# Kernel optimization log

Hardware: AMD Instinct MI355X
Metric: run time of the kernel (lower is better)

Reference implementation:

```python
import jax, jax.numpy as jnp
import numpy as np

N_NODES = 50000
N_EDGES = 400000
D = 64        # hidden_features
H_NE = 16     # hidden_ne_features
L = 4         # num_layers
EPS = 1e-5


def _ln(z, g, b):
    # layer norm over feature dim
    mu = jnp.mean(z, axis=-1, keepdims=True)
    var = jnp.var(z, axis=-1, keepdims=True)
    return (z - mu) * jax.lax.rsqrt(var + EPS) * g + b


def setup_inputs() -> dict:
    key = jax.random.key(0)
    ks = iter(jax.random.split(key, 64))
    def rn(shape, s=0.05):
        return jax.random.normal(next(ks), shape, dtype=jnp.float32) * s
    inp = {
        "x": rn((N_NODES, 2), 1.0),
        "e": rn((N_EDGES, 2), 1.0),
        "src": jax.random.randint(next(ks), (N_EDGES,), 0, N_NODES, dtype=jnp.int32),
        "dst": jax.random.randint(next(ks), (N_EDGES,), 0, N_NODES, dtype=jnp.int32),
        # node / edge encoders (2-layer MLPs)
        "ne_W1": rn((2, H_NE)), "ne_b1": jnp.zeros((H_NE,), jnp.float32),
        "ne_W2": rn((H_NE, D)), "ne_b2": jnp.zeros((D,), jnp.float32),
        "ee_W1": rn((2, H_NE)), "ee_b1": jnp.zeros((H_NE,), jnp.float32),
        "ee_W2": rn((H_NE, D)), "ee_b2": jnp.zeros((D,), jnp.float32),
        # stacked per-layer GatedGCN weights
        "A1": rn((L, D, D)), "bA1": jnp.zeros((L, D), jnp.float32),
        "A2": rn((L, D, D)), "bA2": jnp.zeros((L, D), jnp.float32),
        "A3": rn((L, D, D)), "bA3": jnp.zeros((L, D), jnp.float32),
        "B1": rn((L, D, D)), "bB1": jnp.zeros((L, D), jnp.float32),
        "B2": rn((L, D, D)), "bB2": jnp.zeros((L, D), jnp.float32),
        "B3": rn((L, D, D)), "bB3": jnp.zeros((L, D), jnp.float32),
        "ge": jnp.ones((L, D), jnp.float32), "be": jnp.zeros((L, D), jnp.float32),
        "gh": jnp.ones((L, D), jnp.float32), "bh": jnp.zeros((L, D), jnp.float32),
        # score predictor
        "pW1": rn((3 * D, D)), "pb1": jnp.zeros((D,), jnp.float32),
        "pW2": rn((D, 1)), "pb2": jnp.zeros((1,), jnp.float32),
    }
    return inp


def _forward(x, e, src, dst,
             ne_W1, ne_b1, ne_W2, ne_b2,
             ee_W1, ee_b1, ee_W2, ee_b2,
             A1, bA1, A2, bA2, A3, bA3,
             B1, bB1, B2, bB2, B3, bB3,
             ge, be, gh, bh,
             pW1, pb1, pW2, pb2):
    # encoders
    x = jax.nn.relu(x @ ne_W1 + ne_b1) @ ne_W2 + ne_b2      # [N, D]
    e = jax.nn.relu(e @ ee_W1 + ee_b1) @ ee_W2 + ee_b2      # [E, D]

    params = {"A1": A1, "bA1": bA1, "A2": A2, "bA2": bA2,
              "A3": A3, "bA3": bA3, "B1": B1, "bB1": bB1,
              "B2": B2, "bB2": bB2, "B3": B3, "bB3": bB3,
              "ge": ge, "be": be, "gh": gh, "bh": bh}

    def layer(carry, p):
        x, e = carry
        # edge update: e_ij += ReLU(LN(B1 h_i + B2 h_j + B3 e_ij))
        e_hat = (x[src] @ p["B1"] + p["bB1"]
                 + x[dst] @ p["B2"] + p["bB2"]
                 + e @ p["B3"] + p["bB3"])                  # [E, D]
        e = e + jax.nn.relu(_ln(e_hat, p["ge"], p["be"]))
        sigma = jax.nn.sigmoid(e)                             # gates [E, D]
        # directed aggregation: forward (src->dst) and backward (dst->src)
        a2 = x @ p["A2"] + p["bA2"]
        a3 = x @ p["A3"] + p["bA3"]
        m_f = jax.ops.segment_sum(sigma * a2[src], dst, num_segments=N_NODES)
        d_f = jax.ops.segment_sum(sigma, dst, num_segments=N_NODES)
        m_b = jax.ops.segment_sum(sigma * a3[dst], src, num_segments=N_NODES)
        d_b = jax.ops.segment_sum(sigma, src, num_segments=N_NODES)
        h = (x @ p["A1"] + p["bA1"]
             + m_f / (d_f + EPS) + m_b / (d_b + EPS))        # [N, D]
        x = x + jax.nn.relu(_ln(h, p["gh"], p["bh"]))
        return (x, e), None

    (x, e), _ = jax.lax.scan(layer, (x, e), params)

    # score predictor: MLP over cat(x_src, x_dst, e)
    z = jnp.concatenate([x[src], x[dst], e], axis=-1)        # [E, 3D]
    return jax.nn.relu(z @ pW1 + pb1) @ pW2 + pb2            # [E, 1]


def reference(x, e, src, dst,
              ne_W1, ne_b1, ne_W2, ne_b2,
              ee_W1, ee_b1, ee_W2, ee_b2,
              A1, bA1, A2, bA2, A3, bA3,
              B1, bB1, B2, bB2, B3, bB3,
              ge, be, gh, bh,
              pW1, pb1, pW2, pb2):
    return _forward(x, e, src, dst,
                    ne_W1, ne_b1, ne_W2, ne_b2,
                    ee_W1, ee_b1, ee_W2, ee_b2,
                    A1, bA1, A2, bA2, A3, bA3,
                    B1, bB1, B2, bB2, B3, bB3,
                    ge, be, gh, bh,
                    pW1, pb1, pW2, pb2)
```

## Files before the change

### kernel.cpp

```cpp
#include <hip/hip_runtime.h>

#define N_NODES 50000
#define N_EDGES 400000
#define EPSV 1e-5f
#define SCAN_BLK 49
#define SCAN_PAD (49 * 1024)

__global__ __launch_bounds__(256) void encode_kernel(
    const float* __restrict__ in2, const float* __restrict__ W1,
    const float* __restrict__ b1, const float* __restrict__ W2,
    const float* __restrict__ b2, float* __restrict__ out, int nrows)
{
  int t = blockIdx.x * 256 + threadIdx.x;
  int row = t >> 4;
  int d0 = t & 15;
  if (row >= nrows) return;
  float x0 = in2[row * 2 + 0], x1 = in2[row * 2 + 1];
  float h[16];
#pragma unroll
  for (int j = 0; j < 16; ++j)
    h[j] = fmaxf(fmaf(x0, W1[j], fmaf(x1, W1[16 + j], b1[j])), 0.f);
#pragma unroll
  for (int q = 0; q < 4; ++q) {
    int d = d0 + q * 16;
    float a = b2[d];
#pragma unroll
    for (int j = 0; j < 16; ++j) a = fmaf(h[j], W2[j * 64 + d], a);
    out[(size_t)row * 64 + d] = a;
  }
}

__global__ __launch_bounds__(256) void encode_perm_kernel(
    const float* __restrict__ in2, const float* __restrict__ W1,
    const float* __restrict__ b1, const float* __restrict__ W2,
    const float* __restrict__ b2, const int2* __restrict__ csr_f,
    float* __restrict__ out)
{
  int t = blockIdx.x * 256 + threadIdx.x;
  int row = t >> 4;
  int d0 = t & 15;
  if (row >= N_EDGES) return;
  int orig = csr_f[row].x;
  float x0 = in2[orig * 2 + 0], x1 = in2[orig * 2 + 1];
  float h[16];
#pragma unroll
  for (int j = 0; j < 16; ++j)
    h[j] = fmaxf(fmaf(x0, W1[j], fmaf(x1, W1[16 + j], b1[j])), 0.f);
#pragma unroll
  for (int q = 0; q < 4; ++q) {
    int d = d0 + q * 16;
    float a = b2[d];
#pragma unroll
    for (int j = 0; j < 16; ++j) a = fmaf(h[j], W2[j * 64 + d], a);
    out[(size_t)row * 64 + d] = a;
  }
}

__global__ __launch_bounds__(256) void hist_kernel(
    const int* __restrict__ src, const int* __restrict__ dst,
    int* __restrict__ cnt_f, int* __restrict__ cnt_b)
{
  int t = blockIdx.x * 256 + threadIdx.x;
  if (t >= N_EDGES) return;
  atomicAdd(&cnt_f[dst[t]], 1);
  atomicAdd(&cnt_b[src[t]], 1);
}

__global__ __launch_bounds__(1024) void scanA_kernel(
    const int* __restrict__ cnt_f, const int* __restrict__ cnt_b,
    int* __restrict__ part, int* __restrict__ bsum)
{
  int dir = blockIdx.x / SCAN_BLK;
  int blk = blockIdx.x % SCAN_BLK;
  const int* cnt = dir ? cnt_b : cnt_f;
  int t = threadIdx.x;
  int idx = blk * 1024 + t;
  int v = (idx < N_NODES) ? cnt[idx] : 0;
  __shared__ int sh[1024];
  sh[t] = v;
  __syncthreads();
  for (int o = 1; o < 1024; o <<= 1) {
    int u = (t >= o) ? sh[t - o] : 0;
    __syncthreads();
    sh[t] += u;
    __syncthreads();
  }
  part[dir * SCAN_PAD + idx] = sh[t] - v;
  if (t == 1023) bsum[dir * SCAN_BLK + blk] = sh[1023];
}

__global__ __launch_bounds__(128) void scanB_kernel(
    int* __restrict__ bsum, int* __restrict__ off_f, int* __restrict__ off_b)
{
  int dir = threadIdx.x >> 6;
  int i = threadIdx.x & 63;
  int v = (i < SCAN_BLK) ? bsum[dir * SCAN_BLK + i] : 0;
  int s = v;
#pragma unroll
  for (int o = 1; o < 64; o <<= 1) {
    int u = __shfl_up(s, o, 64);
    if (i >= o) s += u;
  }
  if (i < SCAN_BLK) bsum[dir * SCAN_BLK + i] = s - v;
  if (i == SCAN_BLK - 1) {
    if (dir == 0) off_f[N_NODES] = s;
    else off_b[N_NODES] = s;
  }
}

__global__ __launch_bounds__(1024) void scanC_kernel(
    const int* __restrict__ part, const int* __restrict__ bsum,
    int* __restrict__ off_f, int* __restrict__ off_b,
    int* __restrict__ cur_f, int* __restrict__ cur_b)
{
  int dir = blockIdx.x / SCAN_BLK;
  int blk = blockIdx.x % SCAN_BLK;
  int t = threadIdx.x;
  int idx = blk * 1024 + t;
  if (idx >= N_NODES) return;
  int v = part[dir * SCAN_PAD + idx] + bsum[dir * SCAN_BLK + blk];
  if (dir == 0) { off_f[idx] = v; cur_f[idx] = v; }
  else { off_b[idx] = v; cur_b[idx] = v; }
}

__global__ __launch_bounds__(256) void fill_kernel(
    const int* __restrict__ src, const int* __restrict__ dst,
    int* __restrict__ cur_f, int* __restrict__ cur_b,
    int2* __restrict__ csr_f, int2* __restrict__ csr_b)
{
  int t = blockIdx.x * 256 + threadIdx.x;
  if (t >= N_EDGES) return;
  int dv = dst[t], sv = src[t];
  int p = atomicAdd(&cur_f[dv], 1);
  csr_f[p] = make_int2(t, sv);
  int q = atomicAdd(&cur_b[sv], 1);
  csr_b[q] = make_int2(t, dv);
}

__global__ __launch_bounds__(256) void sort_kernel(
    const int* __restrict__ off_f, const int* __restrict__ off_b,
    int2* __restrict__ csr_f, int2* __restrict__ csr_b)
{
  int t = blockIdx.x * 256 + threadIdx.x;
  int n;
  int2* csr;
  const int* off;
  if (t < N_NODES) { n = t; csr = csr_f; off = off_f; }
  else if (t < 2 * N_NODES) { n = t - N_NODES; csr = csr_b; off = off_b; }
  else return;
  int b = off[n], e = off[n + 1];
  for (int i = b + 1; i < e; ++i) {
    int2 key = csr[i];
    int j = i - 1;
    while (j >= b && csr[j].x > key.x) { csr[j + 1] = csr[j]; --j; }
    csr[j + 1] = key;
  }
}

__global__ __launch_bounds__(256) void aux_inv_kernel(
    const int2* __restrict__ csr_f, int* __restrict__ inv_f,
    int* __restrict__ src_f)
{
  int p = blockIdx.x * 256 + threadIdx.x;
  if (p >= N_EDGES) return;
  int2 c = csr_f[p];
  inv_f[c.x] = p;
  src_f[p] = c.y;
}

__global__ __launch_bounds__(256) void aux_dst_kernel(
    const int* __restrict__ off_f, int* __restrict__ dst_f)
{
  int n = blockIdx.x * 256 + threadIdx.x;
  if (n >= N_NODES) return;
  int b = off_f[n], e = off_f[n + 1];
  for (int p = b; p < e; ++p) dst_f[p] = n;
}

__global__ __launch_bounds__(256) void aux_remap_kernel(
    const int* __restrict__ inv_f, int2* __restrict__ csr_b)
{
  int q = blockIdx.x * 256 + threadIdx.x;
  if (q >= N_EDGES) return;
  int2 c = csr_b[q];
  csr_b[q] = make_int2(inv_f[c.x], c.y);
}


__global__ __launch_bounds__(320, 6) void node_gemm_kernel(
    const float* __restrict__ X,
    const float* __restrict__ A1, const float* __restrict__ A2,
    const float* __restrict__ A3, const float* __restrict__ B1,
    const float* __restrict__ B2,
    const float* __restrict__ bA1, const float* __restrict__ bA2,
    const float* __restrict__ bA3, const float* __restrict__ bB1,
    const float* __restrict__ bB2,
    float* __restrict__ NA, int l)
{
  __shared__ float tl[64 * 36];
  int wid = threadIdx.x >> 6;
  int lane = threadIdx.x & 63;
  int row0 = blockIdx.x * 32;
  for (int i = threadIdx.x; i < 32 * 16; i += 320) {
    int r = i >> 4, c4 = (i & 15) * 4;
    int row = row0 + r;
    float4 v = (row < N_NODES)
                   ? *reinterpret_cast<const float4*>(&X[(size_t)row * 64 + c4])
                   : make_float4(0.f, 0.f, 0.f, 0.f);
    tl[(c4 + 0) * 36 + r] = v.x;
    tl[(c4 + 1) * 36 + r] = v.y;
    tl[(c4 + 2) * 36 + r] = v.z;
    tl[(c4 + 3) * 36 + r] = v.w;
  }
  __syncthreads();
  int r8 = lane & 7, c8 = lane >> 3;
  int col = 8 * c8;
  const float* W;
  const float* bb;
  if (wid == 0) { W = A1; bb = bA1; }
  else if (wid == 1) { W = A2; bb = bA2; }
  else if (wid == 2) { W = A3; bb = bA3; }
  else if (wid == 3) { W = B1; bb = bB1; }
  else { W = B2; bb = bB2; }
  W += l * 64 * 64;
  float acc[4][8];
#pragma unroll
  for (int i = 0; i < 4; ++i)
#pragma unroll
    for (int j = 0; j < 8; ++j) acc[i][j] = 0.f;
#pragma unroll 8
  for (int k = 0; k < 64; ++k) {
    float4 er = *reinterpret_cast<const float4*>(&tl[k * 36 + 4 * r8]);
    float4 w0 = *reinterpret_cast<const float4*>(&W[k * 64 + col]);
    float4 w1 = *reinterpret_cast<const float4*>(&W[k * 64 + col + 4]);
    float ev[4] = {er.x, er.y, er.z, er.w};
    float wv[8] = {w0.x, w0.y, w0.z, w0.w, w1.x, w1.y, w1.z, w1.w};
#pragma unroll
    for (int i = 0; i < 4; ++i)
#pragma unroll
      for (int j = 0; j < 8; ++j) acc[i][j] = fmaf(ev[i], wv[j], acc[i][j]);
  }
  float4 b0 = *reinterpret_cast<const float4*>(&bb[l * 64 + col]);
  float4 b1 = *reinterpret_cast<const float4*>(&bb[l * 64 + col + 4]);
  float* out = NA + (size_t)wid * N_NODES * 64;
#pragma unroll
  for (int i = 0; i < 4; ++i) {
    int row = row0 + 4 * r8 + i;
    if (row < N_NODES) {
      *reinterpret_cast<float4*>(&out[(size_t)row * 64 + col]) =
          make_float4(acc[i][0] + b0.x, acc[i][1] + b0.y, acc[i][2] + b0.z,
                      acc[i][3] + b0.w);
      *reinterpret_cast<float4*>(&out[(size_t)row * 64 + col + 4]) =
          make_float4(acc[i][4] + b1.x, acc[i][5] + b1.y, acc[i][6] + b1.z,
                      acc[i][7] + b1.w);
    }
  }
}

__global__ __launch_bounds__(256, 8) void edge_update_kernel(
    const float* __restrict__ NA,
    const float* __restrict__ B3, const float* __restrict__ bB3,
    const float* __restrict__ ge, const float* __restrict__ be,
    const int* __restrict__ src_f, const int* __restrict__ dst_f,
    float* __restrict__ E64, int l)
{
  __shared__ float ett[4][64 * 20];
  int wid = threadIdx.x >> 6;
  int lane = threadIdx.x & 63;
  int tile = blockIdx.x * 4 + wid;
  int e0 = tile * 16;
  int r4 = lane & 3, c16 = lane >> 2;
  int col = 4 * c16;
  float* tl = ett[wid];
#pragma unroll
  for (int rb = 0; rb < 4; ++rb) {
    int r = e0 + 4 * rb;
    float v0 = E64[(size_t)(r + 0) * 64 + lane];
    float v1 = E64[(size_t)(r + 1) * 64 + lane];
    float v2 = E64[(size_t)(r + 2) * 64 + lane];
    float v3 = E64[(size_t)(r + 3) * 64 + lane];
    *reinterpret_cast<float4*>(&tl[lane * 20 + 4 * rb]) =
        make_float4(v0, v1, v2, v3);
  }
  const float* W = B3 + l * 64 * 64;
  float acc[4][4];
#pragma unroll
  for (int i = 0; i < 4; ++i)
#pragma unroll
    for (int j = 0; j < 4; ++j) acc[i][j] = 0.f;
#pragma unroll 8
  for (int k = 0; k < 64; ++k) {
    float4 er = *reinterpret_cast<const float4*>(&tl[k * 20 + 4 * r4]);
    float4 w0 = *reinterpret_cast<const float4*>(&W[k * 64 + col]);
    float ev[4] = {er.x, er.y, er.z, er.w};
    float wv[4] = {w0.x, w0.y, w0.z, w0.w};
#pragma unroll
    for (int i = 0; i < 4; ++i)
#pragma unroll
      for (int j = 0; j < 4; ++j) acc[i][j] = fmaf(ev[i], wv[j], acc[i][j]);
  }
  const float* b1x = NA + (size_t)3 * N_NODES * 64;
  const float* b2x = NA + (size_t)4 * N_NODES * 64;
  float4 t0;
  t0 = *reinterpret_cast<const float4*>(&bB3[l * 64 + col]);
  float bbv[4] = {t0.x, t0.y, t0.z, t0.w};
  t0 = *reinterpret_cast<const float4*>(&ge[l * 64 + col]);
  float gev[4] = {t0.x, t0.y, t0.z, t0.w};
  t0 = *reinterpret_cast<const float4*>(&be[l * 64 + col]);
  float bev[4] = {t0.x, t0.y, t0.z, t0.w};
#pragma unroll
  for (int i = 0; i < 4; ++i) {
    int row = e0 + 4 * r4 + i;
    int sv = src_f[row];
    int dv = dst_f[row];
    float4 g0 = *reinterpret_cast<const float4*>(&b1x[(size_t)sv * 64 + col]);
    float4 h0 = *reinterpret_cast<const float4*>(&b2x[(size_t)dv * 64 + col]);
    float4 o0 = *reinterpret_cast<const float4*>(&E64[(size_t)row * 64 + col]);
    float g1v[4] = {g0.x, g0.y, g0.z, g0.w};
    float g2v[4] = {h0.x, h0.y, h0.z, h0.w};
    float eov[4] = {o0.x, o0.y, o0.z, o0.w};
    float z[4];
    float s1 = 0.f, s2 = 0.f;
#pragma unroll
    for (int j = 0; j < 4; ++j) {
      z[j] = acc[i][j] + bbv[j] + g1v[j] + g2v[j];
      s1 += z[j];
      s2 = fmaf(z[j], z[j], s2);
    }
    s1 += __shfl_xor(s1, 4, 64);  s2 += __shfl_xor(s2, 4, 64);
    s1 += __shfl_xor(s1, 8, 64);  s2 += __shfl_xor(s2, 8, 64);
    s1 += __shfl_xor(s1, 16, 64); s2 += __shfl_xor(s2, 16, 64);
    s1 += __shfl_xor(s1, 32, 64); s2 += __shfl_xor(s2, 32, 64);
    float mean = s1 * (1.f / 64.f);
    float var = fmaxf(s2 * (1.f / 64.f) - mean * mean, 0.f);
    float rstd = rsqrtf(var + EPSV);
    float o[4];
#pragma unroll
    for (int j = 0; j < 4; ++j)
      o[j] = eov[j] + fmaxf(fmaf((z[j] - mean) * rstd, gev[j], bev[j]), 0.f);
    *reinterpret_cast<float4*>(&E64[(size_t)row * 64 + col]) =
        make_float4(o[0], o[1], o[2], o[3]);
  }
}

__global__ __launch_bounds__(256) void aggregate_kernel(
    const float* __restrict__ NA, const float* __restrict__ E64,
    const int* __restrict__ off_f, const int* __restrict__ off_b,
    const int* __restrict__ src_f, const int2* __restrict__ csr_b,
    const float* __restrict__ gh, const float* __restrict__ bh,
    float* __restrict__ X, int l)
{
  int wave = threadIdx.x >> 6;
  int lane = threadIdx.x & 63;
  int n = blockIdx.x * 4 + wave;
  if (n >= N_NODES) return;
  const float* A1x = NA;
  const float* A2x = NA + (size_t)N_NODES * 64;
  const float* A3x = NA + (size_t)2 * N_NODES * 64;
  float xo = X[(size_t)n * 64 + lane];
  float a1v = A1x[(size_t)n * 64 + lane];
  float ghv = gh[l * 64 + lane];
  float bhv = bh[l * 64 + lane];
  int pf = off_f[n], pfe = off_f[n + 1];
  int pb = off_b[n], pbe = off_b[n + 1];
  float mf = 0.f, df = 0.f, mb = 0.f, db = 0.f;
#pragma unroll 4
  for (int p = pf; p < pfe; ++p) {
    float ev = E64[(size_t)p * 64 + lane];
    float av = A2x[(size_t)src_f[p] * 64 + lane];
    float sg = __builtin_amdgcn_rcpf(1.f + __expf(-ev));
    mf = fmaf(sg, av, mf);
    df += sg;
  }
#pragma unroll 4
  for (int p = pb; p < pbe; ++p) {
    int2 c = csr_b[p];
    float ev = E64[(size_t)c.x * 64 + lane];
    float av = A3x[(size_t)c.y * 64 + lane];
    float sg = __builtin_amdgcn_rcpf(1.f + __expf(-ev));
    mb = fmaf(sg, av, mb);
    db += sg;
  }
  float h = a1v + mf * __builtin_amdgcn_rcpf(df + EPSV) +
            mb * __builtin_amdgcn_rcpf(db + EPSV);
  float s1 = h, s2 = h * h;
#pragma unroll
  for (int m = 1; m < 64; m <<= 1) {
    s1 += __shfl_xor(s1, m, 64);
    s2 += __shfl_xor(s2, m, 64);
  }
  float mean = s1 * (1.f / 64.f);
  float var = fmaxf(s2 * (1.f / 64.f) - mean * mean, 0.f);
  float rstd = rsqrtf(var + EPSV);
  X[(size_t)n * 64 + lane] =
      xo + fmaxf(fmaf((h - mean) * rstd, ghv, bhv), 0.f);
}

__global__ __launch_bounds__(128, 8) void pred_node_kernel(
    const float* __restrict__ X, const float* __restrict__ pW1,
    float* __restrict__ U, float* __restrict__ V)
{
  __shared__ float tl[64 * 36];
  int wid = threadIdx.x >> 6;
  int lane = threadIdx.x & 63;
  int row0 = blockIdx.x * 32;
  for (int i = threadIdx.x; i < 32 * 16; i += 128) {
    int r = i >> 4, c4 = (i & 15) * 4;
    int row = row0 + r;
    float4 v = (row < N_NODES)
                   ? *reinterpret_cast<const float4*>(&X[(size_t)row * 64 + c4])
                   : make_float4(0.f, 0.f, 0.f, 0.f);
    tl[(c4 + 0) * 36 + r] = v.x;
    tl[(c4 + 1) * 36 + r] = v.y;
    tl[(c4 + 2) * 36 + r] = v.z;
    tl[(c4 + 3) * 36 + r] = v.w;
  }
  __syncthreads();
  int r8 = lane & 7, c8 = lane >> 3;
  int col = 8 * c8;
  const float* W = pW1 + (size_t)wid * 64 * 64;
  float acc[4][8];
#pragma unroll
  for (int i = 0; i < 4; ++i)
#pragma unroll
    for (int j = 0; j < 8; ++j) acc[i][j] = 0.f;
#pragma unroll 8
  for (int k = 0; k < 64; ++k) {
    float4 er = *reinterpret_cast<const float4*>(&tl[k * 36 + 4 * r8]);
    float4 w0 = *reinterpret_cast<const float4*>(&W[k * 64 + col]);
    float4 w1 = *reinterpret_cast<const float4*>(&W[k * 64 + col + 4]);
    float ev[4] = {er.x, er.y, er.z, er.w};
    float wv[8] = {w0.x, w0.y, w0.z, w0.w, w1.x, w1.y, w1.z, w1.w};
#pragma unroll
    for (int i = 0; i < 4; ++i)
#pragma unroll
      for (int j = 0; j < 8; ++j) acc[i][j] = fmaf(ev[i], wv[j], acc[i][j]);
  }
  float* out = wid ? V : U;
#pragma unroll
  for (int i = 0; i < 4; ++i) {
    int row = row0 + 4 * r8 + i;
    if (row < N_NODES) {
      *reinterpret_cast<float4*>(&out[(size_t)row * 64 + col]) =
          make_float4(acc[i][0], acc[i][1], acc[i][2], acc[i][3]);
      *reinterpret_cast<float4*>(&out[(size_t)row * 64 + col + 4]) =
          make_float4(acc[i][4], acc[i][5], acc[i][6], acc[i][7]);
    }
  }
}

__global__ __launch_bounds__(256, 8) void pred_edge_kernel(
    const float* __restrict__ U, const float* __restrict__ V,
    const float* __restrict__ E64,
    const int2* __restrict__ csr_f, const int* __restrict__ dst_f,
    const float* __restrict__ pW1, const float* __restrict__ pb1,
    const float* __restrict__ pW2, const float* __restrict__ pb2,
    float* __restrict__ out)
{
  __shared__ float ett[4][64 * 20];
  int wid = threadIdx.x >> 6;
  int lane = threadIdx.x & 63;
  int tile = blockIdx.x * 4 + wid;
  int e0 = tile * 16;
  int r4 = lane & 3, c16 = lane >> 2;
  int col = 4 * c16;
  float* tl = ett[wid];
#pragma unroll
  for (int rb = 0; rb < 4; ++rb) {
    int r = e0 + 4 * rb;
    float v0 = E64[(size_t)(r + 0) * 64 + lane];
    float v1 = E64[(size_t)(r + 1) * 64 + lane];
    float v2 = E64[(size_t)(r + 2) * 64 + lane];
    float v3 = E64[(size_t)(r + 3) * 64 + lane];
    *reinterpret_cast<float4*>(&tl[lane * 20 + 4 * rb]) =
        make_float4(v0, v1, v2, v3);
  }
  const float* W = pW1 + (size_t)128 * 64;
  float acc[4][4];
#pragma unroll
  for (int i = 0; i < 4; ++i)
#pragma unroll
    for (int j = 0; j < 4; ++j) acc[i][j] = 0.f;
#pragma unroll 8
  for (int k = 0; k < 64; ++k) {
    float4 er = *reinterpret_cast<const float4*>(&tl[k * 20 + 4 * r4]);
    float4 w0 = *reinterpret_cast<const float4*>(&W[k * 64 + col]);
    float ev[4] = {er.x, er.y, er.z, er.w};
    float wv[4] = {w0.x, w0.y, w0.z, w0.w};
#pragma unroll
    for (int i = 0; i < 4; ++i)
#pragma unroll
      for (int j = 0; j < 4; ++j) acc[i][j] = fmaf(ev[i], wv[j], acc[i][j]);
  }
  float4 t0;
  t0 = *reinterpret_cast<const float4*>(&pb1[col]);
  float pb1v[4] = {t0.x, t0.y, t0.z, t0.w};
  t0 = *reinterpret_cast<const float4*>(&pW2[col]);
  float pw2v[4] = {t0.x, t0.y, t0.z, t0.w};
  float pb2v = pb2[0];
#pragma unroll
  for (int i = 0; i < 4; ++i) {
    int row = e0 + 4 * r4 + i;
    int2 cf = csr_f[row];
    int sv = cf.y;
    int dv = dst_f[row];
    float4 g0 = *reinterpret_cast<const float4*>(&U[(size_t)sv * 64 + col]);
    float4 h0 = *reinterpret_cast<const float4*>(&V[(size_t)dv * 64 + col]);
    float g1v[4] = {g0.x, g0.y, g0.z, g0.w};
    float g2v[4] = {h0.x, h0.y, h0.z, h0.w};
    float hsum = 0.f;
#pragma unroll
    for (int j = 0; j < 4; ++j) {
      float z = acc[i][j] + pb1v[j] + g1v[j] + g2v[j];
      hsum = fmaf(fmaxf(z, 0.f), pw2v[j], hsum);
    }
    hsum += __shfl_xor(hsum, 4, 64);
    hsum += __shfl_xor(hsum, 8, 64);
    hsum += __shfl_xor(hsum, 16, 64);
    hsum += __shfl_xor(hsum, 32, 64);
    if (c16 == 0) out[cf.x] = hsum + pb2v;
  }
}

extern "C" void kernel_launch(void* const* d_in, const int* in_sizes, int n_in,
                              void* d_out, int out_size, void* d_ws, size_t ws_size,
                              hipStream_t stream)
{
  const float* x = (const float*)d_in[0];
  const float* e = (const float*)d_in[1];
  const int* src = (const int*)d_in[2];
  const int* dst = (const int*)d_in[3];
  const float* neW1 = (const float*)d_in[4];
  const float* neb1 = (const float*)d_in[5];
  const float* neW2 = (const float*)d_in[6];
  const float* neb2 = (const float*)d_in[7];
  const float* eeW1 = (const float*)d_in[8];
  const float* eeb1 = (const float*)d_in[9];
  const float* eeW2 = (const float*)d_in[10];
  const float* eeb2 = (const float*)d_in[11];
  const float* A1 = (const float*)d_in[12];
  const float* bA1 = (const float*)d_in[13];
  const float* A2 = (const float*)d_in[14];
  const float* bA2 = (const float*)d_in[15];
  const float* A3 = (const float*)d_in[16];
  const float* bA3 = (const float*)d_in[17];
  const float* B1 = (const float*)d_in[18];
  const float* bB1 = (const float*)d_in[19];
  const float* B2 = (const float*)d_in[20];
  const float* bB2 = (const float*)d_in[21];
  const float* B3 = (const float*)d_in[22];
  const float* bB3 = (const float*)d_in[23];
  const float* ge = (const float*)d_in[24];
  const float* be = (const float*)d_in[25];
  const float* gh = (const float*)d_in[26];
  const float* bh = (const float*)d_in[27];
  const float* pW1 = (const float*)d_in[28];
  const float* pb1 = (const float*)d_in[29];
  const float* pW2 = (const float*)d_in[30];
  const float* pb2 = (const float*)d_in[31];

  char* ws = (char*)d_ws;
  float* X = (float*)ws;      ws += (size_t)N_NODES * 64 * 4;
  float* NA = (float*)ws;     ws += (size_t)5 * N_NODES * 64 * 4;
  float* E64 = (float*)ws;    ws += (size_t)N_EDGES * 64 * 4;
  int* cnt_f = (int*)ws;      ws += (size_t)N_NODES * 4;
  int* cnt_b = (int*)ws;      ws += (size_t)N_NODES * 4;
  int* off_f = (int*)ws;      ws += (size_t)(N_NODES + 1) * 4;
  int* off_b = (int*)ws;      ws += (size_t)(N_NODES + 1) * 4;
  int* cur_f = (int*)ws;      ws += (size_t)N_NODES * 4;
  int* cur_b = (int*)ws;      ws += (size_t)N_NODES * 4;
  int2* csr_f = (int2*)ws;    ws += (size_t)N_EDGES * 8;
  int2* csr_b = (int2*)ws;    ws += (size_t)N_EDGES * 8;
  int* part = (int*)ws;       ws += (size_t)2 * SCAN_PAD * 4;
  int* bsum = (int*)ws;       ws += (size_t)2 * SCAN_BLK * 4;
  int* inv_f = (int*)ws;      ws += (size_t)N_EDGES * 4;
  int* dst_f = (int*)ws;      ws += (size_t)N_EDGES * 4;
  int* src_f = (int*)ws;      ws += (size_t)N_EDGES * 4;
  float* U = NA + (size_t)3 * N_NODES * 64;
  float* V = NA + (size_t)4 * N_NODES * 64;

  hipMemsetAsync(cnt_f, 0, (size_t)2 * N_NODES * 4, stream);
  hist_kernel<<<(N_EDGES + 255) / 256, 256, 0, stream>>>(src, dst, cnt_f, cnt_b);
  scanA_kernel<<<2 * SCAN_BLK, 1024, 0, stream>>>(cnt_f, cnt_b, part, bsum);
  scanB_kernel<<<1, 128, 0, stream>>>(bsum, off_f, off_b);
  scanC_kernel<<<2 * SCAN_BLK, 1024, 0, stream>>>(part, bsum, off_f, off_b,
                                                  cur_f, cur_b);
  fill_kernel<<<(N_EDGES + 255) / 256, 256, 0, stream>>>(src, dst, cur_f, cur_b,
                                                         csr_f, csr_b);
  sort_kernel<<<(2 * N_NODES + 255) / 256, 256, 0, stream>>>(off_f, off_b, csr_f,
                                                             csr_b);
  aux_inv_kernel<<<(N_EDGES + 255) / 256, 256, 0, stream>>>(csr_f, inv_f, src_f);
  aux_dst_kernel<<<(N_NODES + 255) / 256, 256, 0, stream>>>(off_f, dst_f);
  aux_remap_kernel<<<(N_EDGES + 255) / 256, 256, 0, stream>>>(inv_f, csr_b);

  encode_kernel<<<(N_NODES * 16 + 255) / 256, 256, 0, stream>>>(
      x, neW1, neb1, neW2, neb2, X, N_NODES);
  encode_perm_kernel<<<(N_EDGES * 16 + 255) / 256, 256, 0, stream>>>(
      e, eeW1, eeb1, eeW2, eeb2, csr_f, E64);

  const int NT = (N_NODES + 31) / 32;
  for (int l = 0; l < 4; ++l) {
    node_gemm_kernel<<<NT, 320, 0, stream>>>(
        X, A1, A2, A3, B1, B2, bA1, bA2, bA3, bB1, bB2, NA, l);
    edge_update_kernel<<<N_EDGES / 64, 256, 0, stream>>>(NA, B3, bB3, ge, be,
                                                         src_f, dst_f, E64, l);
    aggregate_kernel<<<(N_NODES + 3) / 4, 256, 0, stream>>>(
        NA, E64, off_f, off_b, src_f, csr_b, gh, bh, X, l);
  }

  pred_node_kernel<<<NT, 128, 0, stream>>>(X, pW1, U, V);
  pred_edge_kernel<<<N_EDGES / 64, 256, 0, stream>>>(U, V, E64, csr_f, dst_f,
                                                     pW1, pb1, pW2, pb2,
                                                     (float*)d_out);
}
```

Before: 1.150 ms.

## Process four edge tiles per wave with register double-buffered prefetch

The edge update and edge prediction kernels now have each wave loop over four 16-edge tiles. While one tile is being computed, the next tile's edge features and index vectors are loaded into registers. Index loads become vectorized int4 loads, and the node-row gathers are issued before the GEMM loop so their latency overlaps compute. The grid shrinks by four and the occupancy hint drops from 8 to 4, trading register pressure and fewer resident waves for more in-flight memory per wave.

New measurement: 1.444 ms. 25.6% more time.

```diff
diff --git a/kernel.cpp b/kernel.cpp
--- a/kernel.cpp
+++ b/kernel.cpp
@@ -5,6 +5,7 @@
 #define EPSV 1e-5f
 #define SCAN_BLK 49
 #define SCAN_PAD (49 * 1024)
+#define NTILE 25000
 
 __global__ __launch_bounds__(256) void encode_kernel(
     const float* __restrict__ in2, const float* __restrict__ W1,
@@ -186,7 +187,6 @@
   csr_b[q] = make_int2(inv_f[c.x], c.y);
 }
 
-
 __global__ __launch_bounds__(320, 6) void node_gemm_kernel(
     const float* __restrict__ X,
     const float* __restrict__ A1, const float* __restrict__ A2,
@@ -257,7 +257,7 @@
   }
 }
 
-__global__ __launch_bounds__(256, 8) void edge_update_kernel(
+__global__ __launch_bounds__(256, 4) void edge_update_kernel(
     const float* __restrict__ NA,
     const float* __restrict__ B3, const float* __restrict__ bB3,
     const float* __restrict__ ge, const float* __restrict__ be,
@@ -267,79 +267,113 @@
   __shared__ float ett[4][64 * 20];
   int wid = threadIdx.x >> 6;
   int lane = threadIdx.x & 63;
-  int tile = blockIdx.x * 4 + wid;
-  int e0 = tile * 16;
   int r4 = lane & 3, c16 = lane >> 2;
   int col = 4 * c16;
   float* tl = ett[wid];
-#pragma unroll
-  for (int rb = 0; rb < 4; ++rb) {
-    int r = e0 + 4 * rb;
-    float v0 = E64[(size_t)(r + 0) * 64 + lane];
-    float v1 = E64[(size_t)(r + 1) * 64 + lane];
-    float v2 = E64[(size_t)(r + 2) * 64 + lane];
-    float v3 = E64[(size_t)(r + 3) * 64 + lane];
-    *reinterpret_cast<float4*>(&tl[lane * 20 + 4 * rb]) =
-        make_float4(v0, v1, v2, v3);
-  }
   const float* W = B3 + l * 64 * 64;
-  float acc[4][4];
-#pragma unroll
-  for (int i = 0; i < 4; ++i)
-#pragma unroll
-    for (int j = 0; j < 4; ++j) acc[i][j] = 0.f;
-#pragma unroll 8
-  for (int k = 0; k < 64; ++k) {
-    float4 er = *reinterpret_cast<const float4*>(&tl[k * 20 + 4 * r4]);
-    float4 w0 = *reinterpret_cast<const float4*>(&W[k * 64 + col]);
-    float ev[4] = {er.x, er.y, er.z, er.w};
-    float wv[4] = {w0.x, w0.y, w0.z, w0.w};
-#pragma unroll
-    for (int i = 0; i < 4; ++i)
-#pragma unroll
-      for (int j = 0; j < 4; ++j) acc[i][j] = fmaf(ev[i], wv[j], acc[i][j]);
-  }
   const float* b1x = NA + (size_t)3 * N_NODES * 64;
   const float* b2x = NA + (size_t)4 * N_NODES * 64;
-  float4 t0;
-  t0 = *reinterpret_cast<const float4*>(&bB3[l * 64 + col]);
-  float bbv[4] = {t0.x, t0.y, t0.z, t0.w};
-  t0 = *reinterpret_cast<const float4*>(&ge[l * 64 + col]);
-  float gev[4] = {t0.x, t0.y, t0.z, t0.w};
-  t0 = *reinterpret_cast<const float4*>(&be[l * 64 + col]);
-  float bev[4] = {t0.x, t0.y, t0.z, t0.w};
-#pragma unroll
-  for (int i = 0; i < 4; ++i) {
-    int row = e0 + 4 * r4 + i;
-    int sv = src_f[row];
-    int dv = dst_f[row];
-    float4 g0 = *reinterpret_cast<const float4*>(&b1x[(size_t)sv * 64 + col]);
-    float4 h0 = *reinterpret_cast<const float4*>(&b2x[(size_t)dv * 64 + col]);
-    float4 o0 = *reinterpret_cast<const float4*>(&E64[(size_t)row * 64 + col]);
-    float g1v[4] = {g0.x, g0.y, g0.z, g0.w};
-    float g2v[4] = {h0.x, h0.y, h0.z, h0.w};
-    float eov[4] = {o0.x, o0.y, o0.z, o0.w};
-    float z[4];
-    float s1 = 0.f, s2 = 0.f;
-#pragma unroll
-    for (int j = 0; j < 4; ++j) {
-      z[j] = acc[i][j] + bbv[j] + g1v[j] + g2v[j];
-      s1 += z[j];
-      s2 = fmaf(z[j], z[j], s2);
-    }
-    s1 += __shfl_xor(s1, 4, 64);  s2 += __shfl_xor(s2, 4, 64);
-    s1 += __shfl_xor(s1, 8, 64);  s2 += __shfl_xor(s2, 8, 64);
-    s1 += __shfl_xor(s1, 16, 64); s2 += __shfl_xor(s2, 16, 64);
-    s1 += __shfl_xor(s1, 32, 64); s2 += __shfl_xor(s2, 32, 64);
-    float mean = s1 * (1.f / 64.f);
-    float var = fmaxf(s2 * (1.f / 64.f) - mean * mean, 0.f);
-    float rstd = rsqrtf(var + EPSV);
-    float o[4];
-#pragma unroll
-    for (int j = 0; j < 4; ++j)
-      o[j] = eov[j] + fmaxf(fmaf((z[j] - mean) * rstd, gev[j], bev[j]), 0.f);
-    *reinterpret_cast<float4*>(&E64[(size_t)row * 64 + col]) =
-        make_float4(o[0], o[1], o[2], o[3]);
+  float4 tv;
+  tv = *reinterpret_cast<const float4*>(&bB3[l * 64 + col]);
+  float bbv[4] = {tv.x, tv.y, tv.z, tv.w};
+  tv = *reinterpret_cast<const float4*>(&ge[l * 64 + col]);
+  float gev[4] = {tv.x, tv.y, tv.z, tv.w};
+  tv = *reinterpret_cast<const float4*>(&be[l * 64 + col]);
+  float bev[4] = {tv.x, tv.y, tv.z, tv.w};
+
+  int tile0 = (blockIdx.x * 4 + wid) * 4;
+  float sr[2][16];
+  int4 svi[2], dvi[2];
+  if (tile0 < NTILE) {
+    int e0 = tile0 * 16;
+#pragma unroll
+    for (int rb = 0; rb < 4; ++rb) {
+      int r = e0 + 4 * rb;
+      sr[0][4 * rb + 0] = E64[(size_t)(r + 0) * 64 + lane];
+      sr[0][4 * rb + 1] = E64[(size_t)(r + 1) * 64 + lane];
+      sr[0][4 * rb + 2] = E64[(size_t)(r + 2) * 64 + lane];
+      sr[0][4 * rb + 3] = E64[(size_t)(r + 3) * 64 + lane];
+    }
+    svi[0] = *reinterpret_cast<const int4*>(&src_f[e0 + 4 * r4]);
+    dvi[0] = *reinterpret_cast<const int4*>(&dst_f[e0 + 4 * r4]);
+  }
+#pragma unroll
+  for (int tt = 0; tt < 4; ++tt) {
+    int tile = tile0 + tt;
+    if (tile >= NTILE) break;
+    int e0 = tile * 16;
+    int cur = tt & 1, nxt = cur ^ 1;
+#pragma unroll
+    for (int rb = 0; rb < 4; ++rb)
+      *reinterpret_cast<float4*>(&tl[lane * 20 + 4 * rb]) =
+          make_float4(sr[cur][4 * rb + 0], sr[cur][4 * rb + 1],
+                      sr[cur][4 * rb + 2], sr[cur][4 * rb + 3]);
+    if (tt < 3 && tile + 1 < NTILE) {
+      int e1 = (tile + 1) * 16;
+#pragma unroll
+      for (int rb = 0; rb < 4; ++rb) {
+        int r = e1 + 4 * rb;
+        sr[nxt][4 * rb + 0] = E64[(size_t)(r + 0) * 64 + lane];
+        sr[nxt][4 * rb + 1] = E64[(size_t)(r + 1) * 64 + lane];
+        sr[nxt][4 * rb + 2] = E64[(size_t)(r + 2) * 64 + lane];
+        sr[nxt][4 * rb + 3] = E64[(size_t)(r + 3) * 64 + lane];
+      }
+      svi[nxt] = *reinterpret_cast<const int4*>(&src_f[e1 + 4 * r4]);
+      dvi[nxt] = *reinterpret_cast<const int4*>(&dst_f[e1 + 4 * r4]);
+    }
+    int svA[4] = {svi[cur].x, svi[cur].y, svi[cur].z, svi[cur].w};
+    int dvA[4] = {dvi[cur].x, dvi[cur].y, dvi[cur].z, dvi[cur].w};
+    float4 g1[4], g2[4];
+#pragma unroll
+    for (int i = 0; i < 4; ++i) {
+      g1[i] = *reinterpret_cast<const float4*>(&b1x[(size_t)svA[i] * 64 + col]);
+      g2[i] = *reinterpret_cast<const float4*>(&b2x[(size_t)dvA[i] * 64 + col]);
+    }
+    float acc[4][4];
+#pragma unroll
+    for (int i = 0; i < 4; ++i)
+#pragma unroll
+      for (int j = 0; j < 4; ++j) acc[i][j] = 0.f;
+#pragma unroll 8
+    for (int k = 0; k < 64; ++k) {
+      float4 er = *reinterpret_cast<const float4*>(&tl[k * 20 + 4 * r4]);
+      float4 w0 = *reinterpret_cast<const float4*>(&W[k * 64 + col]);
+      float ev[4] = {er.x, er.y, er.z, er.w};
+      float wv[4] = {w0.x, w0.y, w0.z, w0.w};
+#pragma unroll
+      for (int i = 0; i < 4; ++i)
+#pragma unroll
+        for (int j = 0; j < 4; ++j) acc[i][j] = fmaf(ev[i], wv[j], acc[i][j]);
+    }
+#pragma unroll
+    for (int i = 0; i < 4; ++i) {
+      int row = e0 + 4 * r4 + i;
+      float4 o0 = *reinterpret_cast<const float4*>(&E64[(size_t)row * 64 + col]);
+      float g1v[4] = {g1[i].x, g1[i].y, g1[i].z, g1[i].w};
+      float g2v[4] = {g2[i].x, g2[i].y, g2[i].z, g2[i].w};
+      float eov[4] = {o0.x, o0.y, o0.z, o0.w};
+      float z[4];
+      float s1 = 0.f, s2 = 0.f;
+#pragma unroll
+      for (int j = 0; j < 4; ++j) {
+        z[j] = acc[i][j] + bbv[j] + g1v[j] + g2v[j];
+        s1 += z[j];
+        s2 = fmaf(z[j], z[j], s2);
+      }
+      s1 += __shfl_xor(s1, 4, 64);  s2 += __shfl_xor(s2, 4, 64);
+      s1 += __shfl_xor(s1, 8, 64);  s2 += __shfl_xor(s2, 8, 64);
+      s1 += __shfl_xor(s1, 16, 64); s2 += __shfl_xor(s2, 16, 64);
+      s1 += __shfl_xor(s1, 32, 64); s2 += __shfl_xor(s2, 32, 64);
+      float mean = s1 * (1.f / 64.f);
+      float var = fmaxf(s2 * (1.f / 64.f) - mean * mean, 0.f);
+      float rstd = rsqrtf(var + EPSV);
+      float o[4];
+#pragma unroll
+      for (int j = 0; j < 4; ++j)
+        o[j] = eov[j] + fmaxf(fmaf((z[j] - mean) * rstd, gev[j], bev[j]), 0.f);
+      *reinterpret_cast<float4*>(&E64[(size_t)row * 64 + col]) =
+          make_float4(o[0], o[1], o[2], o[3]);
+    }
   }
 }
 
@@ -449,7 +483,7 @@
   }
 }
 
-__global__ __launch_bounds__(256, 8) void pred_edge_kernel(
+__global__ __launch_bounds__(256, 4) void pred_edge_kernel(
     const float* __restrict__ U, const float* __restrict__ V,
     const float* __restrict__ E64,
     const int2* __restrict__ csr_f, const int* __restrict__ dst_f,
@@ -460,65 +494,101 @@
   __shared__ float ett[4][64 * 20];
   int wid = threadIdx.x >> 6;
   int lane = threadIdx.x & 63;
-  int tile = blockIdx.x * 4 + wid;
-  int e0 = tile * 16;
   int r4 = lane & 3, c16 = lane >> 2;
   int col = 4 * c16;
   float* tl = ett[wid];
-#pragma unroll
-  for (int rb = 0; rb < 4; ++rb) {
-    int r = e0 + 4 * rb;
-    float v0 = E64[(size_t)(r + 0) * 64 + lane];
-    float v1 = E64[(size_t)(r + 1) * 64 + lane];
-    float v2 = E64[(size_t)(r + 2) * 64 + lane];
-    float v3 = E64[(size_t)(r + 3) * 64 + lane];
-    *reinterpret_cast<float4*>(&tl[lane * 20 + 4 * rb]) =
-        make_float4(v0, v1, v2, v3);
-  }
   const float* W = pW1 + (size_t)128 * 64;
-  float acc[4][4];
-#pragma unroll
-  for (int i = 0; i < 4; ++i)
-#pragma unroll
-    for (int j = 0; j < 4; ++j) acc[i][j] = 0.f;
+  float4 tv;
+  tv = *reinterpret_cast<const float4*>(&pb1[col]);
+  float pb1v[4] = {tv.x, tv.y, tv.z, tv.w};
+  tv = *reinterpret_cast<const float4*>(&pW2[col]);
+  float pw2v[4] = {tv.x, tv.y, tv.z, tv.w};
+  float pb2v = pb2[0];
+
+  int tile0 = (blockIdx.x * 4 + wid) * 4;
+  float sr[2][16];
+  int4 ca[2], cb[2], dvi[2];
+  if (tile0 < NTILE) {
+    int e0 = tile0 * 16;
+#pragma unroll
+    for (int rb = 0; rb < 4; ++rb) {
+      int r = e0 + 4 * rb;
+      sr[0][4 * rb + 0] = E64[(size_t)(r + 0) * 64 + lane];
+      sr[0][4 * rb + 1] = E64[(size_t)(r + 1) * 64 + lane];
+      sr[0][4 * rb + 2] = E64[(size_t)(r + 2) * 64 + lane];
+      sr[0][4 * rb + 3] = E64[(size_t)(r + 3) * 64 + lane];
+    }
+    ca[0] = *reinterpret_cast<const int4*>(&csr_f[e0 + 4 * r4]);
+    cb[0] = *reinterpret_cast<const int4*>(&csr_f[e0 + 4 * r4 + 2]);
+    dvi[0] = *reinterpret_cast<const int4*>(&dst_f[e0 + 4 * r4]);
+  }
+#pragma unroll
+  for (int tt = 0; tt < 4; ++tt) {
+    int tile = tile0 + tt;
+    if (tile >= NTILE) break;
+    int cur = tt & 1, nxt = cur ^ 1;
+#pragma unroll
+    for (int rb = 0; rb < 4; ++rb)
+      *reinterpret_cast<float4*>(&tl[lane * 20 + 4 * rb]) =
+          make_float4(sr[cur][4 * rb + 0], sr[cur][4 * rb + 1],
+                      sr[cur][4 * rb + 2], sr[cur][4 * rb + 3]);
+    if (tt < 3 && tile + 1 < NTILE) {
+      int e1 = (tile + 1) * 16;
+#pragma unroll
+      for (int rb = 0; rb < 4; ++rb) {
+        int r = e1 + 4 * rb;
+        sr[nxt][4 * rb + 0] = E64[(size_t)(r + 0) * 64 + lane];
+        sr[nxt][4 * rb + 1] = E64[(size_t)(r + 1) * 64 + lane];
+        sr[nxt][4 * rb + 2] = E64[(size_t)(r + 2) * 64 + lane];
+        sr[nxt][4 * rb + 3] = E64[(size_t)(r + 3) * 64 + lane];
+      }
+      ca[nxt] = *reinterpret_cast<const int4*>(&csr_f[e1 + 4 * r4]);
+      cb[nxt] = *reinterpret_cast<const int4*>(&csr_f[e1 + 4 * r4 + 2]);
+      dvi[nxt] = *reinterpret_cast<const int4*>(&dst_f[e1 + 4 * r4]);
+    }
+    int opos[4] = {ca[cur].x, ca[cur].z, cb[cur].x, cb[cur].z};
+    int svA[4] = {ca[cur].y, ca[cur].w, cb[cur].y, cb[cur].w};
+    int dvA[4] = {dvi[cur].x, dvi[cur].y, dvi[cur].z, dvi[cur].w};
+    float4 g1[4], g2[4];
+#pragma unroll
+    for (int i = 0; i < 4; ++i) {
+      g1[i] = *reinterpret_cast<const float4*>(&U[(size_t)svA[i] * 64 + col]);
+      g2[i] = *reinterpret_cast<const float4*>(&V[(size_t)dvA[i] * 64 + col]);
+    }
+    float acc[4][4];
+#pragma unroll
+    for (int i = 0; i < 4; ++i)
+#pragma unroll
+      for (int j = 0; j < 4; ++j) acc[i][j] = 0.f;
 #pragma unroll 8
-  for (int k = 0; k < 64; ++k) {
-    float4 er = *reinterpret_cast<const float4*>(&tl[k * 20 + 4 * r4]);
-    float4 w0 = *reinterpret_cast<const float4*>(&W[k * 64 + col]);
-    float ev[4] = {er.x, er.y, er.z, er.w};
-    float wv[4] = {w0.x, w0.y, w0.z, w0.w};
-#pragma unroll
-    for (int i = 0; i < 4; ++i)
-#pragma unroll
-      for (int j = 0; j < 4; ++j) acc[i][j] = fmaf(ev[i], wv[j], acc[i][j]);
-  }
-  float4 t0;
-  t0 = *reinterpret_cast<const float4*>(&pb1[col]);
-  float pb1v[4] = {t0.x, t0.y, t0.z, t0.w};
-  t0 = *reinterpret_cast<const float4*>(&pW2[col]);
-  float pw2v[4] = {t0.x, t0.y, t0.z, t0.w};
-  float pb2v = pb2[0];
-#pragma unroll
-  for (int i = 0; i < 4; ++i) {
-    int row = e0 + 4 * r4 + i;
-    int2 cf = csr_f[row];
-    int sv = cf.y;
-    int dv = dst_f[row];
-    float4 g0 = *reinterpret_cast<const float4*>(&U[(size_t)sv * 64 + col]);
-    float4 h0 = *reinterpret_cast<const float4*>(&V[(size_t)dv * 64 + col]);
-    float g1v[4] = {g0.x, g0.y, g0.z, g0.w};
-    float g2v[4] = {h0.x, h0.y, h0.z, h0.w};
-    float hsum = 0.f;
-#pragma unroll
-    for (int j = 0; j < 4; ++j) {
-      float z = acc[i][j] + pb1v[j] + g1v[j] + g2v[j];
-      hsum = fmaf(fmaxf(z, 0.f), pw2v[j], hsum);
-    }
-    hsum += __shfl_xor(hsum, 4, 64);
-    hsum += __shfl_xor(hsum, 8, 64);
-    hsum += __shfl_xor(hsum, 16, 64);
-    hsum += __shfl_xor(hsum, 32, 64);
-    if (c16 == 0) out[cf.x] = hsum + pb2v;
+    for (int k = 0; k < 64; ++k) {
+      float4 er = *reinterpret_cast<const float4*>(&tl[k * 20 + 4 * r4]);
+      float4 w0 = *reinterpret_cast<const float4*>(&W[k * 64 + col]);
+      float ev[4] = {er.x, er.y, er.z, er.w};
+      float wv[4] = {w0.x, w0.y, w0.z, w0.w};
+#pragma unroll
+      for (int i = 0; i < 4; ++i)
+#pragma unroll
+        for (int j = 0; j < 4; ++j) acc[i][j] = fmaf(ev[i], wv[j], acc[i][j]);
+    }
+#pragma unroll
+    for (int i = 0; i < 4; ++i) {
+      float hsum = 0.f;
+#pragma unroll
+      for (int j = 0; j < 4; ++j) {
+        float gj = (j == 0) ? g1[i].x : (j == 1) ? g1[i].y : (j == 2) ? g1[i].z
+                                                                     : g1[i].w;
+        float hj = (j == 0) ? g2[i].x : (j == 1) ? g2[i].y : (j == 2) ? g2[i].z
+                                                                     : g2[i].w;
+        float z = acc[i][j] + pb1v[j] + gj + hj;
+        hsum = fmaf(fmaxf(z, 0.f), pw2v[j], hsum);
+      }
+      hsum += __shfl_xor(hsum, 4, 64);
+      hsum += __shfl_xor(hsum, 8, 64);
+      hsum += __shfl_xor(hsum, 16, 64);
+      hsum += __shfl_xor(hsum, 32, 64);
+      if (c16 == 0) out[opos[i]] = hsum + pb2v;
+    }
   }
 }
 
@@ -599,17 +669,18 @@
       e, eeW1, eeb1, eeW2, eeb2, csr_f, E64);
 
   const int NT = (N_NODES + 31) / 32;
+  const int EWB = (NTILE / 4 + 3) / 4;
   for (int l = 0; l < 4; ++l) {
     node_gemm_kernel<<<NT, 320, 0, stream>>>(
         X, A1, A2, A3, B1, B2, bA1, bA2, bA3, bB1, bB2, NA, l);
-    edge_update_kernel<<<N_EDGES / 64, 256, 0, stream>>>(NA, B3, bB3, ge, be,
-                                                         src_f, dst_f, E64, l);
+    edge_update_kernel<<<EWB, 256, 0, stream>>>(NA, B3, bB3, ge, be,
+                                                src_f, dst_f, E64, l);
     aggregate_kernel<<<(N_NODES + 3) / 4, 256, 0, stream>>>(
         NA, E64, off_f, off_b, src_f, csr_b, gh, bh, X, l);
   }
 
   pred_node_kernel<<<NT, 128, 0, stream>>>(X, pW1, U, V);
-  pred_edge_kernel<<<N_EDGES / 64, 256, 0, stream>>>(U, V, E64, csr_f, dst_f,
-                                                     pW1, pb1, pW2, pb2,
-                                                     (float*)d_out);
-}
+  pred_edge_kernel<<<EWB, 256, 0, stream>>>(U, V, E64, csr_f, dst_f,
+                                            pW1, pb1, pW2, pb2,
+                                            (float*)d_out);
+}
```
